# Kernel tuning notes

Hardware: AMD Instinct MI355X
Metric: run time of the kernel (lower is better)

The kernel has to match this reference:

```python
import jax, jax.numpy as jnp
import numpy as np

E, D, H, W = 512, 64, 64, 64
B, L = 8, 2048
STEPS = 5
OUT_SIGMA_SCALE = 2.0


def setup_inputs() -> dict:
    key = jax.random.key(0)
    ks = jax.random.split(key, 8)
    tokens = jax.random.normal(ks[0], (B, L, E), dtype=jnp.float32)
    # positions on the HxW lattice: col 0 in [0,H), col 1 in [0,W)
    pos = jax.random.uniform(ks[1], (B, L, 2), dtype=jnp.float32)
    positions = pos * jnp.array([H, W], dtype=jnp.float32)
    # learned params (fan-in scaled init, as nn.Linear/Conv2d would give)
    W_to_field = jax.random.normal(ks[2], (D, E), dtype=jnp.float32) / np.sqrt(E)
    W_from_field = jax.random.normal(ks[3], (E, D), dtype=jnp.float32) / np.sqrt(D)
    conv1_w = jax.random.normal(ks[4], (2 * D, D, 3, 3), dtype=jnp.float32) / np.sqrt(D * 9)
    conv1_b = jnp.zeros((2 * D,), dtype=jnp.float32)
    conv2_w = jax.random.normal(ks[5], (D, 2 * D, 1, 1), dtype=jnp.float32) / np.sqrt(2 * D)
    conv2_b = jnp.zeros((D,), dtype=jnp.float32)
    log_sigma = jnp.array(np.log(4.0), dtype=jnp.float32)
    return {
        "tokens": tokens, "positions": positions,
        "W_to_field": W_to_field, "W_from_field": W_from_field,
        "conv1_w": conv1_w, "conv1_b": conv1_b,
        "conv2_w": conv2_w, "conv2_b": conv2_b,
        "log_sigma": log_sigma,
    }


def _conv2d(x, w, b, pad):
    y = jax.lax.conv_general_dilated(
        x, w, window_strides=(1, 1), padding=[(pad, pad), (pad, pad)],
        dimension_numbers=("NCHW", "OIHW", "NCHW"))
    return y + b[None, :, None, None]


def _norm_gauss(dy2, dx2, sigma):
    # (B,L,H,1)+(B,L,1,W) -> (B,L,H,W), normalized over the lattice
    g = jnp.exp(-(dy2 + dx2) / (2.0 * sigma * sigma))
    return g / (jnp.sum(g, axis=(-2, -1), keepdims=True) + 1e-6)


def reference(tokens, positions, W_to_field, W_from_field,
              conv1_w, conv1_b, conv2_w, conv2_b, log_sigma):
    sigma_in = jax.nn.softplus(log_sigma) + 1e-6
    sigma_out = sigma_in * OUT_SIGMA_SCALE

    proj = jnp.einsum("ble,de->bld", tokens, W_to_field)  # (B,L,D)

    grid_y = jnp.arange(H, dtype=jnp.float32)  # (H,)
    grid_x = jnp.arange(W, dtype=jnp.float32)  # (W,)
    dy2 = (grid_y[None, None, :, None] - positions[..., 0][..., None, None]) ** 2  # (B,L,H,1)
    dx2 = (grid_x[None, None, None, :] - positions[..., 1][..., None, None]) ** 2  # (B,L,1,W)

    weights_in = _norm_gauss(dy2, dx2, sigma_in)   # (B,L,H,W)
    field = jnp.einsum("blc,blhw->bchw", proj, weights_in)  # (B,D,H,W)

    for _ in range(STEPS):
        h = jax.nn.relu(_conv2d(field, conv1_w, conv1_b, pad=1))
        field = field + _conv2d(h, conv2_w, conv2_b, pad=0)

    weights_out = _norm_gauss(dy2, dx2, sigma_out)  # (B,L,H,W)
    sampled = jnp.einsum("bchw,blhw->blc", field, weights_out)  # (B,L,D)

    tokens_out = jnp.einsum("bld,ed->ble", sampled, W_from_field)  # (B,L,E)
    return tokens_out
```

## Files before the change

### kernel.cpp

```cpp
#include <hip/hip_runtime.h>
#include <cmath>
#include <cstddef>

#define BB 8
#define LL 2048
#define EE 512
#define HW 4096

typedef __attribute__((ext_vector_type(8))) short short8;
typedef __attribute__((ext_vector_type(4))) short short4v;
typedef __attribute__((ext_vector_type(4))) float f32x4;

__device__ __forceinline__ int swz(int row, int k, int ldk) {
    int g = (k >> 3) ^ (row & ((ldk >> 3) - 1));
    return row * ldk + (g << 3) + (k & 7);
}
__device__ __forceinline__ unsigned short f2bf(float f) {
    unsigned u = __builtin_bit_cast(unsigned, f);
    return (unsigned short)((u + 0x7FFFu + ((u >> 16) & 1u)) >> 16);
}
__device__ __forceinline__ float bf2f(short s) {
    return __builtin_bit_cast(float, (unsigned)((unsigned short)s) << 16);
}
__device__ __forceinline__ short4v cvt4(float4 v) {
    short4v r;
    r[0] = (short)f2bf(v.x); r[1] = (short)f2bf(v.y);
    r[2] = (short)f2bf(v.z); r[3] = (short)f2bf(v.w);
    return r;
}
#define MFMA16(acc, a, b) acc = __builtin_amdgcn_mfma_f32_16x16x32_bf16(a, b, acc, 0, 0, 0)

__global__ __launch_bounds__(256) void k_reorder(const float* __restrict__ w1,
        const float* __restrict__ w2,
        short* __restrict__ w1b, short* __restrict__ w2b) {
    int i = blockIdx.x * 256 + threadIdx.x;
    if (i < 73728) {
        int c = i & 63, o = (i >> 6) & 127, tap = i >> 13;
        w1b[i] = (short)f2bf(w1[(size_t)o * 576 + c * 9 + tap]);
    }
    if (i < 8192) w2b[i] = (short)f2bf(w2[i]);
}

__global__ __launch_bounds__(256) void k_gauss(const float* __restrict__ pos,
        const float* __restrict__ lsig,
        short* __restrict__ gyiT, short* __restrict__ gxiT,
        short* __restrict__ gyoT, short* __restrict__ gxo) {
    __shared__ float red[4][4][64];
    __shared__ float tile[64 * 65];
    int t = threadIdx.x;
    int ll = t & 63, q = t >> 6;
    int b = blockIdx.y, lt = blockIdx.x;
    int bl = b * LL + lt * 64 + ll;
    float py = pos[(size_t)bl * 2 + 0];
    float px = pos[(size_t)bl * 2 + 1];
    float ls = lsig[0];
    float si = log1pf(expf(ls)) + 1e-6f;
    float so = si * 2.0f;
    float ai = 0.5f / (si * si), ao = 0.5f / (so * so);
    float vyi[16], vxi[16], vyo[16], vxo[16];
    float pyi = 0.f, pxi = 0.f, pyo = 0.f, pxo = 0.f;
    #pragma unroll
    for (int j = 0; j < 16; j++) {
        float g = (float)(q * 16 + j);
        float dy = g - py, dx = g - px;
        float dy2 = dy * dy, dx2 = dx * dx;
        vyi[j] = expf(-dy2 * ai); pyi += vyi[j];
        vxi[j] = expf(-dx2 * ai); pxi += vxi[j];
        vyo[j] = expf(-dy2 * ao); pyo += vyo[j];
        vxo[j] = expf(-dx2 * ao); pxo += vxo[j];
    }
    red[0][q][ll] = pyi; red[1][q][ll] = pxi;
    red[2][q][ll] = pyo; red[3][q][ll] = pxo;
    __syncthreads();
    float syi = red[0][0][ll] + red[0][1][ll] + red[0][2][ll] + red[0][3][ll];
    float sxi = red[1][0][ll] + red[1][1][ll] + red[1][2][ll] + red[1][3][ll];
    float syo = red[2][0][ll] + red[2][1][ll] + red[2][2][ll] + red[2][3][ll];
    float sxo = red[3][0][ll] + red[3][1][ll] + red[3][2][ll] + red[3][3][ll];
    float inv_i = 1.0f / (syi * sxi + 1e-6f);
    float inv_o = 1.0f / (syo * sxo + 1e-6f);
    size_t base = (size_t)b * 64 * LL + lt * 64 + ll;
    #pragma unroll
    for (int j = 0; j < 16; j++) {
        size_t off = base + (size_t)(q * 16 + j) * LL;
        gyiT[off] = (short)f2bf(vyi[j] * inv_i);
        gxiT[off] = (short)f2bf(vxi[j]);
        gyoT[off] = (short)f2bf(vyo[j] * inv_o);
        tile[(q * 16 + j) * 65 + ll] = vxo[j];
    }
    __syncthreads();
    #pragma unroll
    for (int j = 0; j < 16; j++) {
        int i = t + 256 * j;
        int lo = i >> 6, wo = i & 63;
        gxo[((size_t)b * LL + lt * 64 + lo) * 64 + wo] = (short)f2bf(tile[wo * 65 + lo]);
    }
}

__global__ __launch_bounds__(256) void k_proj(const float* __restrict__ tokens,
        const float* __restrict__ wtf, short* __restrict__ projT) {
    __shared__ __align__(16) short At[4096], Bt[4096];
    int t = threadIdx.x, lane = t & 63, wid = t >> 6;
    int blk = blockIdx.x;
    int b = blk >> 5;
    int l0b = (blk & 31) * 64;
    size_t tokbase = ((size_t)b * LL + l0b) * EE;
    f32x4 z = {0.f, 0.f, 0.f, 0.f};
    f32x4 acc[4] = {z, z, z, z};
    float4 pa[4], pb[4];
    #pragma unroll
    for (int j = 0; j < 4; j++) {
        int idx = t + 256 * j;
        int row = idx >> 4, kq = (idx & 15) << 2;
        pa[j] = *(const float4*)&wtf[(size_t)row * EE + kq];
        pb[j] = *(const float4*)&tokens[tokbase + (size_t)row * EE + kq];
    }
    for (int c = 0; c < 8; c++) {
        __syncthreads();
        #pragma unroll
        for (int j = 0; j < 4; j++) {
            int idx = t + 256 * j;
            int row = idx >> 4, kq = (idx & 15) << 2;
            *(short4v*)&At[swz(row, kq, 64)] = cvt4(pa[j]);
            *(short4v*)&Bt[swz(row, kq, 64)] = cvt4(pb[j]);
        }
        __syncthreads();
        if (c < 7) {
            int e0 = (c + 1) * 64;
            #pragma unroll
            for (int j = 0; j < 4; j++) {
                int idx = t + 256 * j;
                int row = idx >> 4, kq = (idx & 15) << 2;
                pa[j] = *(const float4*)&wtf[(size_t)row * EE + e0 + kq];
                pb[j] = *(const float4*)&tokens[tokbase + (size_t)row * EE + e0 + kq];
            }
        }
        int mrow = wid * 16 + (lane & 15);
        #pragma unroll
        for (int ks = 0; ks < 2; ks++) {
            int k0 = ks * 32 + (lane >> 4) * 8;
            short8 a = *(short8*)&At[swz(mrow, k0, 64)];
            #pragma unroll
            for (int n = 0; n < 4; n++) {
                short8 bb = *(short8*)&Bt[swz(n * 16 + (lane & 15), k0, 64)];
                MFMA16(acc[n], a, bb);
            }
        }
    }
    #pragma unroll
    for (int n = 0; n < 4; n++)
        #pragma unroll
        for (int r = 0; r < 4; r++) {
            int d = wid * 16 + ((lane >> 4) << 2) + r;
            int l = l0b + n * 16 + (lane & 15);
            projT[((size_t)b * 64 + d) * LL + l] = (short)f2bf(acc[n][r]);
        }
}

__global__ __launch_bounds__(256) void k_scatter(const short* __restrict__ projT,
        const short* __restrict__ gyiT, const short* __restrict__ gxiT,
        float* __restrict__ fz) {
    __shared__ __align__(16) char smem[24576];
    short* At = (short*)smem;
    short* B0 = At + 4096;
    short* B1 = B0 + 4096;
    float* Cf = (float*)smem;
    int t = threadIdx.x, lane = t & 63, wid = t >> 6;
    int hp = blockIdx.x, b = blockIdx.y, kz = blockIdx.z;
    int h0 = hp * 2;
    const short* pj  = projT + (size_t)b * 64 * LL + kz * 512;
    const short* gx  = gxiT + (size_t)b * 64 * LL + kz * 512;
    const short* gy0 = gyiT + ((size_t)b * 64 + h0) * LL + kz * 512;
    const short* gy1 = gy0 + LL;
    f32x4 z = {0.f, 0.f, 0.f, 0.f};
    f32x4 acc0[4] = {z, z, z, z}, acc1[4] = {z, z, z, z};
    short8 pA[2], pX[2], pY0[2], pY1[2];
    #pragma unroll
    for (int j = 0; j < 2; j++) {
        int i = t + 256 * j; int row = i >> 3, g = i & 7;
        pA[j]  = *(const short8*)&pj[(size_t)row * LL + g * 8];
        pX[j]  = *(const short8*)&gx[(size_t)row * LL + g * 8];
        pY0[j] = *(const short8*)&gy0[g * 8];
        pY1[j] = *(const short8*)&gy1[g * 8];
    }
    for (int c = 0; c < 8; c++) {
        __syncthreads();
        #pragma unroll
        for (int j = 0; j < 2; j++) {
            int i = t + 256 * j; int row = i >> 3, g = i & 7;
            short8 b0v, b1v;
            #pragma unroll
            for (int e = 0; e < 8; e++) {
                float gxv = bf2f(pX[j][e]);
                b0v[e] = (short)f2bf(gxv * bf2f(pY0[j][e]));
                b1v[e] = (short)f2bf(gxv * bf2f(pY1[j][e]));
            }
            *(short8*)&At[swz(row, g * 8, 64)] = pA[j];
            *(short8*)&B0[swz(row, g * 8, 64)] = b0v;
            *(short8*)&B1[swz(row, g * 8, 64)] = b1v;
        }
        __syncthreads();
        if (c < 7) {
            int l0 = (c + 1) * 64;
            #pragma unroll
            for (int j = 0; j < 2; j++) {
                int i = t + 256 * j; int row = i >> 3, g = i & 7;
                pA[j]  = *(const short8*)&pj[(size_t)row * LL + l0 + g * 8];
                pX[j]  = *(const short8*)&gx[(size_t)row * LL + l0 + g * 8];
                pY0[j] = *(const short8*)&gy0[l0 + g * 8];
                pY1[j] = *(const short8*)&gy1[l0 + g * 8];
            }
        }
        int mrow = wid * 16 + (lane & 15);
        #pragma unroll
        for (int ks = 0; ks < 2; ks++) {
            int k0 = ks * 32 + (lane >> 4) * 8;
            short8 a = *(short8*)&At[swz(mrow, k0, 64)];
            #pragma unroll
            for (int n = 0; n < 4; n++) {
                short8 b0f = *(short8*)&B0[swz(n * 16 + (lane & 15), k0, 64)];
                short8 b1f = *(short8*)&B1[swz(n * 16 + (lane & 15), k0, 64)];
                MFMA16(acc0[n], a, b0f);
                MFMA16(acc1[n], a, b1f);
            }
        }
    }
    float* dst = fz + (size_t)kz * 2097152;
    #pragma unroll
    for (int p = 0; p < 2; p++) {
        __syncthreads();
        #pragma unroll
        for (int n = 0; n < 4; n++)
            #pragma unroll
            for (int r = 0; r < 4; r++) {
                int w = n * 16 + (lane & 15);
                int cc = wid * 16 + ((lane >> 4) << 2) + r;
                Cf[w * 68 + cc] = (p == 0) ? acc0[n][r] : acc1[n][r];
            }
        __syncthreads();
        #pragma unroll
        for (int j = 0; j < 4; j++) {
            int i = t + 256 * j;
            int wo = i >> 4, cq = (i & 15) << 2;
            *(float4*)&dst[(((size_t)b * 64 + h0 + p) * 64 + wo) * 64 + cq] =
                *(float4*)&Cf[wo * 68 + cq];
        }
    }
}

__global__ __launch_bounds__(256) void k_redfield(const float* __restrict__ fz,
        float* __restrict__ fA) {
    const size_t FP = 2097152;
    size_t i = ((size_t)blockIdx.x * 256 + threadIdx.x) * 4;
    float4 a = *(const float4*)&fz[i];
    float4 b = *(const float4*)&fz[i + FP];
    float4 c = *(const float4*)&fz[i + 2 * FP];
    float4 d = *(const float4*)&fz[i + 3 * FP];
    float4 r = {a.x + b.x + c.x + d.x, a.y + b.y + c.y + d.y,
                a.z + b.z + c.z + d.z, a.w + b.w + c.w + d.w};
    *(float4*)&fA[i] = r;
}

__global__ __launch_bounds__(256) void k_conv(const float* __restrict__ fin,
        float* __restrict__ fout,
        const short* __restrict__ w1b, const float* __restrict__ b1,
        const short* __restrict__ w2b, const float* __restrict__ b2,
        short* __restrict__ fnchw, int final_step) {
    __shared__ __align__(16) char smem[78336];
    short* halo = (short*)smem;
    short* w1t  = (short*)(smem + 12800);
    short* ht   = (short*)(smem + 45568);
    short* w2s  = (short*)(smem + 61952);
    float* Cf   = (float*)smem;
    int t = threadIdx.x, lane = t & 63, wid = t >> 6;
    int tile = blockIdx.x, b = blockIdx.y;
    int y0 = (tile >> 3) << 3, x0 = (tile & 7) << 3;
    const float* fb = fin + (size_t)b * 64 * HW;

    for (int i = t; i < 1600; i += 256) {
        int pix = i >> 4, cq = (i & 15) << 2;
        int pr = pix / 10, pc = pix - pr * 10;
        int gy = y0 + pr - 1, gx = x0 + pc - 1;
        float4 v = {0.f, 0.f, 0.f, 0.f};
        if ((unsigned)gy < 64u && (unsigned)gx < 64u)
            v = *(const float4*)&fb[((size_t)gy * 64 + gx) * 64 + cq];
        *(short4v*)&halo[swz(pix, cq, 64)] = cvt4(v);
    }
    for (int i = t; i < 1024; i += 256) {
        int d = i >> 4, g = i & 15;
        short8 v = *(const short8*)&w2b[(size_t)d * 128 + g * 8];
        *(short8*)&w2s[swz(d, g * 8, 128)] = v;
    }
    #pragma unroll
    for (int j = 0; j < 4; j++) {
        int i = t + 256 * j; int o = i >> 3, g = i & 7;
        *(short8*)&w1t[swz(o, g * 8, 64)] = *(const short8*)&w1b[(size_t)o * 64 + g * 8];
    }
    f32x4 accH[8];
    #pragma unroll
    for (int n = 0; n < 8; n++) {
        float bv = b1[n * 16 + (lane & 15)];
        f32x4 v = {bv, bv, bv, bv};
        accH[n] = v;
    }
    __syncthreads();
    short8 w1pf[4];
    #pragma unroll
    for (int j = 0; j < 4; j++) {
        int i = t + 256 * j; int o = i >> 3, g = i & 7;
        w1pf[j] = *(const short8*)&w1b[((size_t)128 + o) * 64 + g * 8];
    }
    int mpix = wid * 16 + (lane & 15);
    int ppy = mpix >> 3, ppx = mpix & 7;

    #pragma unroll
    for (int tap = 0; tap < 9; tap++) {
        short* buf = w1t + (tap & 1) * 8192;
        if (tap < 8) {
            short* nbuf = w1t + ((tap + 1) & 1) * 8192;
            #pragma unroll
            for (int j = 0; j < 4; j++) {
                int i = t + 256 * j; int o = i >> 3, g = i & 7;
                *(short8*)&nbuf[swz(o, g * 8, 64)] = w1pf[j];
            }
            if (tap < 7) {
                #pragma unroll
                for (int j = 0; j < 4; j++) {
                    int i = t + 256 * j; int o = i >> 3, g = i & 7;
                    w1pf[j] = *(const short8*)&w1b[((size_t)(tap + 2) * 128 + o) * 64 + g * 8];
                }
            }
        }
        int ky = tap / 3, kx = tap - ky * 3;
        int hpix = (ppy + ky) * 10 + (ppx + kx);
        #pragma unroll
        for (int ks = 0; ks < 2; ks++) {
            int k0 = ks * 32 + (lane >> 4) * 8;
            short8 a = *(short8*)&halo[swz(hpix, k0, 64)];
            #pragma unroll
            for (int n = 0; n < 8; n++) {
                short8 bb = *(short8*)&buf[swz(n * 16 + (lane & 15), k0, 64)];
                MFMA16(accH[n], a, bb);
            }
        }
        __syncthreads();
    }
    #pragma unroll
    for (int n = 0; n < 8; n++)
        #pragma unroll
        for (int r = 0; r < 4; r++) {
            int m = wid * 16 + ((lane >> 4) << 2) + r;
            int o = n * 16 + (lane & 15);
            ht[swz(m, o, 128)] = (short)f2bf(fmaxf(accH[n][r], 0.f));
        }
    __syncthreads();
    f32x4 acc2[4];
    #pragma unroll
    for (int n = 0; n < 4; n++) {
        float bv = b2[n * 16 + (lane & 15)];
        f32x4 v = {bv, bv, bv, bv};
        acc2[n] = v;
    }
    #pragma unroll
    for (int ks = 0; ks < 4; ks++) {
        int k0 = ks * 32 + (lane >> 4) * 8;
        short8 a = *(short8*)&ht[swz(mpix, k0, 128)];
        #pragma unroll
        for (int n = 0; n < 4; n++) {
            short8 bb = *(short8*)&w2s[swz(n * 16 + (lane & 15), k0, 128)];
            MFMA16(acc2[n], a, bb);
        }
    }
    float* fo = fout + (size_t)b * 64 * HW;
    #pragma unroll
    for (int n = 0; n < 4; n++)
        #pragma unroll
        for (int r = 0; r < 4; r++) {
            int m = wid * 16 + ((lane >> 4) << 2) + r;
            int py = m >> 3, px = m & 7;
            int d = n * 16 + (lane & 15);
            size_t addr = (((size_t)(y0 + py)) * 64 + x0 + px) * 64 + d;
            float val = acc2[n][r] + fb[addr];
            if (!final_step) fo[addr] = val;
            else Cf[d * 68 + m] = val;
        }
    if (final_step) {
        __syncthreads();
        #pragma unroll
        for (int j = 0; j < 4; j++) {
            int i = t + 256 * j;
            int d = i >> 4, pq = (i & 15) << 2;
            int py = pq >> 3, px = pq & 7;
            float4 v = *(float4*)&Cf[d * 68 + pq];
            *(short4v*)&fnchw[(((size_t)b * 64 + d) * 64 + y0 + py) * 64 + x0 + px] =
                cvt4(v);
        }
    }
}

__global__ __launch_bounds__(256) void k_gather(const short* __restrict__ fnchw,
        const short* __restrict__ gyoT, const short* __restrict__ gxo,
        float* __restrict__ sampz) {
    __shared__ __align__(16) short At[4096], Bt[4096];
    int t = threadIdx.x, lane = t & 63, wid = t >> 6;
    int lt = blockIdx.x, b = blockIdx.y, zz = blockIdx.z;
    int l0 = lt * 64;
    f32x4 z4 = {0.f, 0.f, 0.f, 0.f};
    f32x4 acc[4] = {z4, z4, z4, z4};
    short8 pX[2], pF[2];
    float gyv[2];
    #pragma unroll
    for (int j = 0; j < 2; j++) {
        int i = t + 256 * j; int row = i >> 3, g = i & 7;
        pX[j] = *(const short8*)&gxo[((size_t)b * LL + l0 + row) * 64 + g * 8];
    }
    int h0 = zz * 16;
    #pragma unroll
    for (int j = 0; j < 2; j++) {
        int i = t + 256 * j; int row = i >> 3, g = i & 7;
        gyv[j] = bf2f(gyoT[((size_t)b * 64 + h0) * LL + l0 + row]);
        pF[j] = *(const short8*)&fnchw[(((size_t)b * 64 + row) * 64 + h0) * 64 + g * 8];
    }
    for (int c = 0; c < 16; c++) {
        __syncthreads();
        #pragma unroll
        for (int j = 0; j < 2; j++) {
            int i = t + 256 * j; int row = i >> 3, g = i & 7;
            short8 a;
            #pragma unroll
            for (int e = 0; e < 8; e++)
                a[e] = (short)f2bf(bf2f(pX[j][e]) * gyv[j]);
            *(short8*)&At[swz(row, g * 8, 64)] = a;
            *(short8*)&Bt[swz(row, g * 8, 64)] = pF[j];
        }
        __syncthreads();
        if (c < 15) {
            int h = h0 + c + 1;
            #pragma unroll
            for (int j = 0; j < 2; j++) {
                int i = t + 256 * j; int row = i >> 3, g = i & 7;
                gyv[j] = bf2f(gyoT[((size_t)b * 64 + h) * LL + l0 + row]);
                pF[j] = *(const short8*)&fnchw[(((size_t)b * 64 + row) * 64 + h) * 64 + g * 8];
            }
        }
        int mrow = wid * 16 + (lane & 15);
        #pragma unroll
        for (int ks = 0; ks < 2; ks++) {
            int k0 = ks * 32 + (lane >> 4) * 8;
            short8 a = *(short8*)&At[swz(mrow, k0, 64)];
            #pragma unroll
            for (int n = 0; n < 4; n++) {
                short8 bb = *(short8*)&Bt[swz(n * 16 + (lane & 15), k0, 64)];
                MFMA16(acc[n], a, bb);
            }
        }
    }
    #pragma unroll
    for (int n = 0; n < 4; n++)
        #pragma unroll
        for (int r = 0; r < 4; r++) {
            int lr = wid * 16 + ((lane >> 4) << 2) + r;
            int cc = n * 16 + (lane & 15);
            sampz[(((size_t)zz * BB + b) * LL + l0 + lr) * 64 + cc] = acc[n][r];
        }
}

__global__ __launch_bounds__(256) void k_out(const float* __restrict__ samp,
        const float* __restrict__ wff, float* __restrict__ out) {
    __shared__ __align__(16) short At[4096], Bt[4096];
    const size_t SP = 1048576;
    int t = threadIdx.x, lane = t & 63, wid = t >> 6;
    int mt = blockIdx.x, e0 = blockIdx.y * 64;
    #pragma unroll
    for (int j = 0; j < 4; j++) {
        int idx = t + 256 * j;
        int row = idx >> 4, kq = (idx & 15) << 2;
        size_t off = ((size_t)mt * 64 + row) * 64 + kq;
        float4 v0 = *(const float4*)&samp[off];
        float4 v1 = *(const float4*)&samp[off + SP];
        float4 v2 = *(const float4*)&samp[off + 2 * SP];
        float4 v3 = *(const float4*)&samp[off + 3 * SP];
        float4 vs = {v0.x + v1.x + v2.x + v3.x, v0.y + v1.y + v2.y + v3.y,
                     v0.z + v1.z + v2.z + v3.z, v0.w + v1.w + v2.w + v3.w};
        *(short4v*)&At[swz(row, kq, 64)] = cvt4(vs);
        float4 wv = *(const float4*)&wff[(size_t)(e0 + row) * 64 + kq];
        *(short4v*)&Bt[swz(row, kq, 64)] = cvt4(wv);
    }
    __syncthreads();
    f32x4 z = {0.f, 0.f, 0.f, 0.f};
    f32x4 acc[4] = {z, z, z, z};
    int mrow = wid * 16 + (lane & 15);
    #pragma unroll
    for (int ks = 0; ks < 2; ks++) {
        int k0 = ks * 32 + (lane >> 4) * 8;
        short8 a = *(short8*)&At[swz(mrow, k0, 64)];
        #pragma unroll
        for (int n = 0; n < 4; n++) {
            short8 bb = *(short8*)&Bt[swz(n * 16 + (lane & 15), k0, 64)];
            MFMA16(acc[n], a, bb);
        }
    }
    #pragma unroll
    for (int n = 0; n < 4; n++)
        #pragma unroll
        for (int r = 0; r < 4; r++) {
            int lr = wid * 16 + ((lane >> 4) << 2) + r;
            int ec = e0 + n * 16 + (lane & 15);
            out[((size_t)mt * 64 + lr) * EE + ec] = acc[n][r];
        }
}

extern "C" void kernel_launch(void* const* d_in, const int* in_sizes, int n_in,
                              void* d_out, int out_size, void* d_ws, size_t ws_size,
                              hipStream_t stream) {
    const float* tokens = (const float*)d_in[0];
    const float* pos    = (const float*)d_in[1];
    const float* wtf    = (const float*)d_in[2];
    const float* wff    = (const float*)d_in[3];
    const float* w1     = (const float*)d_in[4];
    const float* b1     = (const float*)d_in[5];
    const float* w2     = (const float*)d_in[6];
    const float* b2     = (const float*)d_in[7];
    const float* lsig   = (const float*)d_in[8];
    float* out = (float*)d_out;

    const size_t M1 = 1048576;
    float* ws    = (float*)d_ws;
    short* sbase = (short*)d_ws;
    short* gyiT  = sbase;
    short* gxiT  = sbase + 1 * M1;
    short* gyoT  = sbase + 2 * M1;
    short* gxo   = sbase + 3 * M1;
    short* projT = sbase + 4 * M1;
    float* fz    = ws + 3 * M1;
    float* fA    = ws + 11 * M1;
    float* fB    = ws + 13 * M1;
    short* fnchw = (short*)(ws + 15 * M1);
    float* samp  = ws + 16 * M1;
    short* w1b   = (short*)(ws + 20 * M1);
    short* w2b   = w1b + 73728;

    hipLaunchKernelGGL(k_reorder, dim3(288), dim3(256), 0, stream, w1, w2, w1b, w2b);
    hipLaunchKernelGGL(k_gauss, dim3(32, 8), dim3(256), 0, stream,
                       pos, lsig, gyiT, gxiT, gyoT, gxo);
    hipLaunchKernelGGL(k_proj, dim3(256), dim3(256), 0, stream, tokens, wtf, projT);
    hipLaunchKernelGGL(k_scatter, dim3(32, 8, 4), dim3(256), 0, stream,
                       projT, gyiT, gxiT, fz);
    hipLaunchKernelGGL(k_redfield, dim3(2048), dim3(256), 0, stream, fz, fA);
    const float* ci = fA;
    float* co = fB;
    for (int s = 0; s < 5; s++) {
        hipLaunchKernelGGL(k_conv, dim3(64, 8), dim3(256), 0, stream,
                           ci, co, w1b, b1, w2b, b2, fnchw, (s == 4) ? 1 : 0);
        float* tmp = co; co = (float*)ci; ci = tmp;
    }
    hipLaunchKernelGGL(k_gather, dim3(32, 8, 4), dim3(256), 0, stream,
                       fnchw, gyoT, gxo, samp);
    hipLaunchKernelGGL(k_out, dim3(256, 8), dim3(256), 0, stream,
                       samp, wff, out);
}
```

Before: 244.1 us.

## Fuse weight reorder and split reduction into neighbors, widen scatter/gather K tiles

Folds the weight reorder into k_gauss via extra blocks, and drops the separate split-K reduction kernel by having the first conv sum the partial fields while loading its halo and residual. The scatter and gather kernels now use 128-wide K tiles, so scatter needs only two split-K partials. The conv kernel keeps the 1x1 conv weights in registers and single-buffers the 3x3 tap weights with a barrier per tap, which cuts LDS so three blocks fit per CU. These changes remove launches and a full-field round trip, at the cost of more registers and extra synchronisation.

```diff
diff --git a/kernel.cpp b/kernel.cpp
--- a/kernel.cpp
+++ b/kernel.cpp
@@ -30,26 +30,27 @@
 }
 #define MFMA16(acc, a, b) acc = __builtin_amdgcn_mfma_f32_16x16x32_bf16(a, b, acc, 0, 0, 0)
 
-__global__ __launch_bounds__(256) void k_reorder(const float* __restrict__ w1,
-        const float* __restrict__ w2,
-        short* __restrict__ w1b, short* __restrict__ w2b) {
-    int i = blockIdx.x * 256 + threadIdx.x;
-    if (i < 73728) {
-        int c = i & 63, o = (i >> 6) & 127, tap = i >> 13;
-        w1b[i] = (short)f2bf(w1[(size_t)o * 576 + c * 9 + tap]);
-    }
-    if (i < 8192) w2b[i] = (short)f2bf(w2[i]);
-}
-
 __global__ __launch_bounds__(256) void k_gauss(const float* __restrict__ pos,
         const float* __restrict__ lsig,
         short* __restrict__ gyiT, short* __restrict__ gxiT,
-        short* __restrict__ gyoT, short* __restrict__ gxo) {
+        short* __restrict__ gyoT, short* __restrict__ gxo,
+        const float* __restrict__ w1, const float* __restrict__ w2,
+        short* __restrict__ w1b, short* __restrict__ w2b) {
     __shared__ float red[4][4][64];
     __shared__ float tile[64 * 65];
     int t = threadIdx.x;
+    int bx = blockIdx.x;
+    {
+        int i = bx * 256 + t;
+        if (i < 73728) {
+            int c = i & 63, o = (i >> 6) & 127, tap = i >> 13;
+            w1b[i] = (short)f2bf(w1[(size_t)o * 576 + c * 9 + tap]);
+        }
+        if (i < 8192) w2b[i] = (short)f2bf(w2[i]);
+    }
+    if (bx >= 256) return;
     int ll = t & 63, q = t >> 6;
-    int b = blockIdx.y, lt = blockIdx.x;
+    int b = bx >> 5, lt = bx & 31;
     int bl = b * LL + lt * 64 + ll;
     float py = pos[(size_t)bl * 2 + 0];
     float px = pos[(size_t)bl * 2 + 1];
@@ -156,75 +157,77 @@
         }
 }
 
-__global__ __launch_bounds__(256) void k_scatter(const short* __restrict__ projT,
+__global__ __launch_bounds__(256, 3) void k_scatter(const short* __restrict__ projT,
         const short* __restrict__ gyiT, const short* __restrict__ gxiT,
         float* __restrict__ fz) {
-    __shared__ __align__(16) char smem[24576];
+    __shared__ __align__(16) char smem[49152];
     short* At = (short*)smem;
-    short* B0 = At + 4096;
-    short* B1 = B0 + 4096;
+    short* B0 = At + 8192;
+    short* B1 = B0 + 8192;
     float* Cf = (float*)smem;
+    const size_t FP = (size_t)BB * 64 * HW;
     int t = threadIdx.x, lane = t & 63, wid = t >> 6;
     int hp = blockIdx.x, b = blockIdx.y, kz = blockIdx.z;
     int h0 = hp * 2;
-    const short* pj  = projT + (size_t)b * 64 * LL + kz * 512;
-    const short* gx  = gxiT + (size_t)b * 64 * LL + kz * 512;
-    const short* gy0 = gyiT + ((size_t)b * 64 + h0) * LL + kz * 512;
+    const short* pj  = projT + (size_t)b * 64 * LL + kz * 1024;
+    const short* gx  = gxiT + (size_t)b * 64 * LL + kz * 1024;
+    const short* gy0 = gyiT + ((size_t)b * 64 + h0) * LL + kz * 1024;
     const short* gy1 = gy0 + LL;
     f32x4 z = {0.f, 0.f, 0.f, 0.f};
     f32x4 acc0[4] = {z, z, z, z}, acc1[4] = {z, z, z, z};
-    short8 pA[2], pX[2], pY0[2], pY1[2];
-    #pragma unroll
-    for (int j = 0; j < 2; j++) {
-        int i = t + 256 * j; int row = i >> 3, g = i & 7;
-        pA[j]  = *(const short8*)&pj[(size_t)row * LL + g * 8];
-        pX[j]  = *(const short8*)&gx[(size_t)row * LL + g * 8];
-        pY0[j] = *(const short8*)&gy0[g * 8];
-        pY1[j] = *(const short8*)&gy1[g * 8];
+    int row_ = t >> 4, g_ = t & 15;
+    short8 pA[4], pX[4], pY0v, pY1v;
+    pY0v = *(const short8*)&gy0[g_ * 8];
+    pY1v = *(const short8*)&gy1[g_ * 8];
+    #pragma unroll
+    for (int j = 0; j < 4; j++) {
+        int row = row_ + 16 * j;
+        pA[j] = *(const short8*)&pj[(size_t)row * LL + g_ * 8];
+        pX[j] = *(const short8*)&gx[(size_t)row * LL + g_ * 8];
     }
     for (int c = 0; c < 8; c++) {
         __syncthreads();
         #pragma unroll
-        for (int j = 0; j < 2; j++) {
-            int i = t + 256 * j; int row = i >> 3, g = i & 7;
+        for (int j = 0; j < 4; j++) {
+            int row = row_ + 16 * j;
             short8 b0v, b1v;
             #pragma unroll
             for (int e = 0; e < 8; e++) {
                 float gxv = bf2f(pX[j][e]);
-                b0v[e] = (short)f2bf(gxv * bf2f(pY0[j][e]));
-                b1v[e] = (short)f2bf(gxv * bf2f(pY1[j][e]));
-            }
-            *(short8*)&At[swz(row, g * 8, 64)] = pA[j];
-            *(short8*)&B0[swz(row, g * 8, 64)] = b0v;
-            *(short8*)&B1[swz(row, g * 8, 64)] = b1v;
+                b0v[e] = (short)f2bf(gxv * bf2f(pY0v[e]));
+                b1v[e] = (short)f2bf(gxv * bf2f(pY1v[e]));
+            }
+            *(short8*)&At[swz(row, g_ * 8, 128)] = pA[j];
+            *(short8*)&B0[swz(row, g_ * 8, 128)] = b0v;
+            *(short8*)&B1[swz(row, g_ * 8, 128)] = b1v;
         }
         __syncthreads();
         if (c < 7) {
-            int l0 = (c + 1) * 64;
-            #pragma unroll
-            for (int j = 0; j < 2; j++) {
-                int i = t + 256 * j; int row = i >> 3, g = i & 7;
-                pA[j]  = *(const short8*)&pj[(size_t)row * LL + l0 + g * 8];
-                pX[j]  = *(const short8*)&gx[(size_t)row * LL + l0 + g * 8];
-                pY0[j] = *(const short8*)&gy0[l0 + g * 8];
-                pY1[j] = *(const short8*)&gy1[l0 + g * 8];
+            int off = (c + 1) * 128;
+            pY0v = *(const short8*)&gy0[off + g_ * 8];
+            pY1v = *(const short8*)&gy1[off + g_ * 8];
+            #pragma unroll
+            for (int j = 0; j < 4; j++) {
+                int row = row_ + 16 * j;
+                pA[j] = *(const short8*)&pj[(size_t)row * LL + off + g_ * 8];
+                pX[j] = *(const short8*)&gx[(size_t)row * LL + off + g_ * 8];
             }
         }
         int mrow = wid * 16 + (lane & 15);
         #pragma unroll
-        for (int ks = 0; ks < 2; ks++) {
+        for (int ks = 0; ks < 4; ks++) {
             int k0 = ks * 32 + (lane >> 4) * 8;
-            short8 a = *(short8*)&At[swz(mrow, k0, 64)];
+            short8 a = *(short8*)&At[swz(mrow, k0, 128)];
             #pragma unroll
             for (int n = 0; n < 4; n++) {
-                short8 b0f = *(short8*)&B0[swz(n * 16 + (lane & 15), k0, 64)];
-                short8 b1f = *(short8*)&B1[swz(n * 16 + (lane & 15), k0, 64)];
+                short8 b0f = *(short8*)&B0[swz(n * 16 + (lane & 15), k0, 128)];
+                short8 b1f = *(short8*)&B1[swz(n * 16 + (lane & 15), k0, 128)];
                 MFMA16(acc0[n], a, b0f);
                 MFMA16(acc1[n], a, b1f);
             }
         }
     }
-    float* dst = fz + (size_t)kz * 2097152;
+    float* dst = fz + (size_t)kz * FP;
     #pragma unroll
     for (int p = 0; p < 2; p++) {
         __syncthreads();
@@ -247,53 +250,49 @@
     }
 }
 
-__global__ __launch_bounds__(256) void k_redfield(const float* __restrict__ fz,
-        float* __restrict__ fA) {
-    const size_t FP = 2097152;
-    size_t i = ((size_t)blockIdx.x * 256 + threadIdx.x) * 4;
-    float4 a = *(const float4*)&fz[i];
-    float4 b = *(const float4*)&fz[i + FP];
-    float4 c = *(const float4*)&fz[i + 2 * FP];
-    float4 d = *(const float4*)&fz[i + 3 * FP];
-    float4 r = {a.x + b.x + c.x + d.x, a.y + b.y + c.y + d.y,
-                a.z + b.z + c.z + d.z, a.w + b.w + c.w + d.w};
-    *(float4*)&fA[i] = r;
-}
-
-__global__ __launch_bounds__(256) void k_conv(const float* __restrict__ fin,
-        float* __restrict__ fout,
+__global__ __launch_bounds__(256, 3) void k_conv(const float* __restrict__ fin,
+        int nparts, float* __restrict__ fout,
         const short* __restrict__ w1b, const float* __restrict__ b1,
         const short* __restrict__ w2b, const float* __restrict__ b2,
         short* __restrict__ fnchw, int final_step) {
-    __shared__ __align__(16) char smem[78336];
+    __shared__ __align__(16) char smem[45568];
     short* halo = (short*)smem;
     short* w1t  = (short*)(smem + 12800);
-    short* ht   = (short*)(smem + 45568);
-    short* w2s  = (short*)(smem + 61952);
+    short* ht   = (short*)(smem + 29184);
     float* Cf   = (float*)smem;
+    const size_t FP = (size_t)BB * 64 * HW;
     int t = threadIdx.x, lane = t & 63, wid = t >> 6;
     int tile = blockIdx.x, b = blockIdx.y;
     int y0 = (tile >> 3) << 3, x0 = (tile & 7) << 3;
     const float* fb = fin + (size_t)b * 64 * HW;
 
+    short8 w2f[4][4];
+    #pragma unroll
+    for (int n = 0; n < 4; n++)
+        #pragma unroll
+        for (int ks = 0; ks < 4; ks++)
+            w2f[n][ks] = *(const short8*)&w2b[(size_t)(n * 16 + (lane & 15)) * 128
+                                              + ks * 32 + (lane >> 4) * 8];
+    short8 pf[4];
+    #pragma unroll
+    for (int j = 0; j < 4; j++) {
+        int i = t + 256 * j; int o = i >> 3, g = i & 7;
+        pf[j] = *(const short8*)&w1b[(size_t)o * 64 + g * 8];
+    }
     for (int i = t; i < 1600; i += 256) {
         int pix = i >> 4, cq = (i & 15) << 2;
         int pr = pix / 10, pc = pix - pr * 10;
         int gy = y0 + pr - 1, gx = x0 + pc - 1;
         float4 v = {0.f, 0.f, 0.f, 0.f};
-        if ((unsigned)gy < 64u && (unsigned)gx < 64u)
-            v = *(const float4*)&fb[((size_t)gy * 64 + gx) * 64 + cq];
+        if ((unsigned)gy < 64u && (unsigned)gx < 64u) {
+            size_t a = ((size_t)gy * 64 + gx) * 64 + cq;
+            v = *(const float4*)&fb[a];
+            for (int p = 1; p < nparts; p++) {
+                float4 u = *(const float4*)&fb[(size_t)p * FP + a];
+                v.x += u.x; v.y += u.y; v.z += u.z; v.w += u.w;
+            }
+        }
         *(short4v*)&halo[swz(pix, cq, 64)] = cvt4(v);
-    }
-    for (int i = t; i < 1024; i += 256) {
-        int d = i >> 4, g = i & 15;
-        short8 v = *(const short8*)&w2b[(size_t)d * 128 + g * 8];
-        *(short8*)&w2s[swz(d, g * 8, 128)] = v;
-    }
-    #pragma unroll
-    for (int j = 0; j < 4; j++) {
-        int i = t + 256 * j; int o = i >> 3, g = i & 7;
-        *(short8*)&w1t[swz(o, g * 8, 64)] = *(const short8*)&w1b[(size_t)o * 64 + g * 8];
     }
     f32x4 accH[8];
     #pragma unroll
@@ -302,34 +301,24 @@
         f32x4 v = {bv, bv, bv, bv};
         accH[n] = v;
     }
-    __syncthreads();
-    short8 w1pf[4];
-    #pragma unroll
-    for (int j = 0; j < 4; j++) {
-        int i = t + 256 * j; int o = i >> 3, g = i & 7;
-        w1pf[j] = *(const short8*)&w1b[((size_t)128 + o) * 64 + g * 8];
-    }
     int mpix = wid * 16 + (lane & 15);
     int ppy = mpix >> 3, ppx = mpix & 7;
 
     #pragma unroll
     for (int tap = 0; tap < 9; tap++) {
-        short* buf = w1t + (tap & 1) * 8192;
+        #pragma unroll
+        for (int j = 0; j < 4; j++) {
+            int i = t + 256 * j; int o = i >> 3, g = i & 7;
+            *(short8*)&w1t[swz(o, g * 8, 64)] = pf[j];
+        }
         if (tap < 8) {
-            short* nbuf = w1t + ((tap + 1) & 1) * 8192;
             #pragma unroll
             for (int j = 0; j < 4; j++) {
                 int i = t + 256 * j; int o = i >> 3, g = i & 7;
-                *(short8*)&nbuf[swz(o, g * 8, 64)] = w1pf[j];
-            }
-            if (tap < 7) {
-                #pragma unroll
-                for (int j = 0; j < 4; j++) {
-                    int i = t + 256 * j; int o = i >> 3, g = i & 7;
-                    w1pf[j] = *(const short8*)&w1b[((size_t)(tap + 2) * 128 + o) * 64 + g * 8];
-                }
-            }
-        }
+                pf[j] = *(const short8*)&w1b[((size_t)(tap + 1) * 128 + o) * 64 + g * 8];
+            }
+        }
+        __syncthreads();
         int ky = tap / 3, kx = tap - ky * 3;
         int hpix = (ppy + ky) * 10 + (ppx + kx);
         #pragma unroll
@@ -338,7 +327,7 @@
             short8 a = *(short8*)&halo[swz(hpix, k0, 64)];
             #pragma unroll
             for (int n = 0; n < 8; n++) {
-                short8 bb = *(short8*)&buf[swz(n * 16 + (lane & 15), k0, 64)];
+                short8 bb = *(short8*)&w1t[swz(n * 16 + (lane & 15), k0, 64)];
                 MFMA16(accH[n], a, bb);
             }
         }
@@ -365,10 +354,7 @@
         int k0 = ks * 32 + (lane >> 4) * 8;
         short8 a = *(short8*)&ht[swz(mpix, k0, 128)];
         #pragma unroll
-        for (int n = 0; n < 4; n++) {
-            short8 bb = *(short8*)&w2s[swz(n * 16 + (lane & 15), k0, 128)];
-            MFMA16(acc2[n], a, bb);
-        }
+        for (int n = 0; n < 4; n++) MFMA16(acc2[n], a, w2f[n][ks]);
     }
     float* fo = fout + (size_t)b * 64 * HW;
     #pragma unroll
@@ -378,9 +364,11 @@
             int m = wid * 16 + ((lane >> 4) << 2) + r;
             int py = m >> 3, px = m & 7;
             int d = n * 16 + (lane & 15);
-            size_t addr = (((size_t)(y0 + py)) * 64 + x0 + px) * 64 + d;
-            float val = acc2[n][r] + fb[addr];
-            if (!final_step) fo[addr] = val;
+            size_t a = (((size_t)(y0 + py)) * 64 + x0 + px) * 64 + d;
+            float fv = fb[a];
+            for (int p = 1; p < nparts; p++) fv += fb[(size_t)p * FP + a];
+            float val = acc2[n][r] + fv;
+            if (!final_step) fo[a] = val;
             else Cf[d * 68 + m] = val;
         }
     if (final_step) {
@@ -397,59 +385,57 @@
     }
 }
 
-__global__ __launch_bounds__(256) void k_gather(const short* __restrict__ fnchw,
+__global__ __launch_bounds__(256, 4) void k_gather(const short* __restrict__ fnchw,
         const short* __restrict__ gyoT, const short* __restrict__ gxo,
         float* __restrict__ sampz) {
-    __shared__ __align__(16) short At[4096], Bt[4096];
+    __shared__ __align__(16) short At[8192], Bt[8192];
     int t = threadIdx.x, lane = t & 63, wid = t >> 6;
     int lt = blockIdx.x, b = blockIdx.y, zz = blockIdx.z;
     int l0 = lt * 64;
     f32x4 z4 = {0.f, 0.f, 0.f, 0.f};
     f32x4 acc[4] = {z4, z4, z4, z4};
-    short8 pX[2], pF[2];
-    float gyv[2];
-    #pragma unroll
-    for (int j = 0; j < 2; j++) {
-        int i = t + 256 * j; int row = i >> 3, g = i & 7;
-        pX[j] = *(const short8*)&gxo[((size_t)b * LL + l0 + row) * 64 + g * 8];
-    }
-    int h0 = zz * 16;
-    #pragma unroll
-    for (int j = 0; j < 2; j++) {
-        int i = t + 256 * j; int row = i >> 3, g = i & 7;
-        gyv[j] = bf2f(gyoT[((size_t)b * 64 + h0) * LL + l0 + row]);
-        pF[j] = *(const short8*)&fnchw[(((size_t)b * 64 + row) * 64 + h0) * 64 + g * 8];
-    }
-    for (int c = 0; c < 16; c++) {
-        __syncthreads();
-        #pragma unroll
-        for (int j = 0; j < 2; j++) {
-            int i = t + 256 * j; int row = i >> 3, g = i & 7;
+    int row_ = t >> 4, g_ = t & 15;
+    int hl_ = g_ >> 3, w8_ = (g_ & 7) * 8;
+    short8 pX[4], pB[4];
+    float pY[4];
+    #pragma unroll
+    for (int j = 0; j < 4; j++) {
+        int row = row_ + 16 * j;
+        int h = zz * 16 + hl_;
+        pX[j] = *(const short8*)&gxo[((size_t)b * LL + l0 + row) * 64 + w8_];
+        pY[j] = bf2f(gyoT[((size_t)b * 64 + h) * LL + l0 + row]);
+        pB[j] = *(const short8*)&fnchw[(((size_t)b * 64 + row) * 64 + h) * 64 + w8_];
+    }
+    for (int c = 0; c < 8; c++) {
+        __syncthreads();
+        #pragma unroll
+        for (int j = 0; j < 4; j++) {
+            int row = row_ + 16 * j;
             short8 a;
             #pragma unroll
             for (int e = 0; e < 8; e++)
-                a[e] = (short)f2bf(bf2f(pX[j][e]) * gyv[j]);
-            *(short8*)&At[swz(row, g * 8, 64)] = a;
-            *(short8*)&Bt[swz(row, g * 8, 64)] = pF[j];
-        }
-        __syncthreads();
-        if (c < 15) {
-            int h = h0 + c + 1;
-            #pragma unroll
-            for (int j = 0; j < 2; j++) {
-                int i = t + 256 * j; int row = i >> 3, g = i & 7;
-                gyv[j] = bf2f(gyoT[((size_t)b * 64 + h) * LL + l0 + row]);
-                pF[j] = *(const short8*)&fnchw[(((size_t)b * 64 + row) * 64 + h) * 64 + g * 8];
+                a[e] = (short)f2bf(bf2f(pX[j][e]) * pY[j]);
+            *(short8*)&At[swz(row, g_ * 8, 128)] = a;
+            *(short8*)&Bt[swz(row, g_ * 8, 128)] = pB[j];
+        }
+        __syncthreads();
+        if (c < 7) {
+            int h = zz * 16 + (c + 1) * 2 + hl_;
+            #pragma unroll
+            for (int j = 0; j < 4; j++) {
+                int row = row_ + 16 * j;
+                pY[j] = bf2f(gyoT[((size_t)b * 64 + h) * LL + l0 + row]);
+                pB[j] = *(const short8*)&fnchw[(((size_t)b * 64 + row) * 64 + h) * 64 + w8_];
             }
         }
         int mrow = wid * 16 + (lane & 15);
         #pragma unroll
-        for (int ks = 0; ks < 2; ks++) {
+        for (int ks = 0; ks < 4; ks++) {
             int k0 = ks * 32 + (lane >> 4) * 8;
-            short8 a = *(short8*)&At[swz(mrow, k0, 64)];
+            short8 a = *(short8*)&At[swz(mrow, k0, 128)];
             #pragma unroll
             for (int n = 0; n < 4; n++) {
-                short8 bb = *(short8*)&Bt[swz(n * 16 + (lane & 15), k0, 64)];
+                short8 bb = *(short8*)&Bt[swz(n * 16 + (lane & 15), k0, 128)];
                 MFMA16(acc[n], a, bb);
             }
         }
@@ -532,27 +518,28 @@
     short* gxo   = sbase + 3 * M1;
     short* projT = sbase + 4 * M1;
     float* fz    = ws + 3 * M1;
-    float* fA    = ws + 11 * M1;
-    float* fB    = ws + 13 * M1;
-    short* fnchw = (short*)(ws + 15 * M1);
-    float* samp  = ws + 16 * M1;
-    short* w1b   = (short*)(ws + 20 * M1);
+    float* fA    = ws + 7 * M1;
+    float* fB    = ws + 9 * M1;
+    short* fnchw = (short*)(ws + 11 * M1);
+    float* samp  = ws + 12 * M1;
+    short* w1b   = (short*)(ws + 16 * M1);
     short* w2b   = w1b + 73728;
 
-    hipLaunchKernelGGL(k_reorder, dim3(288), dim3(256), 0, stream, w1, w2, w1b, w2b);
-    hipLaunchKernelGGL(k_gauss, dim3(32, 8), dim3(256), 0, stream,
-                       pos, lsig, gyiT, gxiT, gyoT, gxo);
+    hipLaunchKernelGGL(k_gauss, dim3(288), dim3(256), 0, stream,
+                       pos, lsig, gyiT, gxiT, gyoT, gxo, w1, w2, w1b, w2b);
     hipLaunchKernelGGL(k_proj, dim3(256), dim3(256), 0, stream, tokens, wtf, projT);
-    hipLaunchKernelGGL(k_scatter, dim3(32, 8, 4), dim3(256), 0, stream,
+    hipLaunchKernelGGL(k_scatter, dim3(32, 8, 2), dim3(256), 0, stream,
                        projT, gyiT, gxiT, fz);
-    hipLaunchKernelGGL(k_redfield, dim3(2048), dim3(256), 0, stream, fz, fA);
-    const float* ci = fA;
-    float* co = fB;
-    for (int s = 0; s < 5; s++) {
-        hipLaunchKernelGGL(k_conv, dim3(64, 8), dim3(256), 0, stream,
-                           ci, co, w1b, b1, w2b, b2, fnchw, (s == 4) ? 1 : 0);
-        float* tmp = co; co = (float*)ci; ci = tmp;
-    }
+    hipLaunchKernelGGL(k_conv, dim3(64, 8), dim3(256), 0, stream,
+                       fz, 2, fB, w1b, b1, w2b, b2, fnchw, 0);
+    hipLaunchKernelGGL(k_conv, dim3(64, 8), dim3(256), 0, stream,
+                       fB, 1, fA, w1b, b1, w2b, b2, fnchw, 0);
+    hipLaunchKernelGGL(k_conv, dim3(64, 8), dim3(256), 0, stream,
+                       fA, 1, fB, w1b, b1, w2b, b2, fnchw, 0);
+    hipLaunchKernelGGL(k_conv, dim3(64, 8), dim3(256), 0, stream,
+                       fB, 1, fA, w1b, b1, w2b, b2, fnchw, 0);
+    hipLaunchKernelGGL(k_conv, dim3(64, 8), dim3(256), 0, stream,
+                       fA, 1, fB, w1b, b1, w2b, b2, fnchw, 1);
     hipLaunchKernelGGL(k_gather, dim3(32, 8, 4), dim3(256), 0, stream,
                        fnchw, gyoT, gxo, samp);
     hipLaunchKernelGGL(k_out, dim3(256, 8), dim3(256), 0, stream,
```

Result: no change. 244.1 us (+0.0%).
